# Kernel tuning notes

Measured on AMD Instinct MI355X. Metric: run time of the kernel, lower is better.

Reference implementation:

```python
import jax, jax.numpy as jnp
import numpy as np

CHUNK = 4        # rows per split
IN_F = 72        # 4*6*3 flattened chunk
OUT_F = 1800     # linear output, viewed as (180,5,2)


def setup_inputs() -> dict:
    key = jax.random.key(0)
    k1, k2, k3 = jax.random.split(key, 3)
    N = 262144  # multiple of 4, so torch's zero-padding of the last chunk is a no-op
    x = jax.random.normal(k1, (N, 6, 3), dtype=jnp.float32)
    W = jax.random.normal(k2, (OUT_F, IN_F), dtype=jnp.float32) * (1.0 / np.sqrt(IN_F))
    b = jax.random.normal(k3, (OUT_F,), dtype=jnp.float32) * 0.01
    return {"x": x, "W": W, "b": b}


def reference(x, W, b):
    # Original: for each split of 4 rows of [6,3], pad to (4,6,3), flatten to 72,
    # Linear(72,1800) + ReLU, view (180,5,2); concatenate all chunks.
    # Vectorized: reshape to [n_chunks, 72] and do one batched GEMM.
    n = x.shape[0]
    n_chunks = -(-n // CHUNK)
    pad = n_chunks * CHUNK - n
    if pad:
        x = jnp.concatenate([x, jnp.zeros((pad, 6, 3), dtype=x.dtype)], axis=0)
    flat = x.reshape(n_chunks, IN_F)                       # [C, 72]
    h = jax.nn.relu(jnp.einsum('ci,oi->co', flat, W) + b)  # [C, 1800]
    # torch returns torch.split(cat, 180): equivalent to the concatenated array
    return h.reshape(n_chunks * 180, 5, 2)
```

## Files before the change

### kernel.cpp

```cpp
#include <hip/hip_runtime.h>
#include <hip/hip_bf16.h>


typedef __bf16 bf16;
typedef bf16  bf16x4 __attribute__((ext_vector_type(4)));
typedef bf16  bf16x8 __attribute__((ext_vector_type(8)));
typedef float f32x4  __attribute__((ext_vector_type(4)));

#define KDIM 72
#define LDK  104
#define NDIM 1800
#define BM   64
#define BN   64

__global__ __launch_bounds__(256, 4)
void edges_mlp_kernel(const float* __restrict__ A,
                      const float* __restrict__ W,
                      const float* __restrict__ bias,
                      float* __restrict__ out)
{
    __shared__ bf16 As[BM][LDK];
    __shared__ bf16 Bs[BN][LDK];

    const int t  = threadIdx.x;
    const int n0 = blockIdx.x * BN;
    const int m0 = blockIdx.y * BM;

    for (int idx = t; idx < BM * 3 * 2; idx += 256) {
        int half = idx / (BM * 3);
        int rem  = idx % (BM * 3);
        int r    = rem / 3;
        int part = rem % 3;
        char* base = half ? (char*)&Bs[r][0] : (char*)&As[r][0];
        *(uint4*)(base + KDIM * 2 + part * 16) = make_uint4(0u, 0u, 0u, 0u);
    }

    const float4* A4 = (const float4*)(A + (size_t)m0 * KDIM);
    for (int i = t; i < BM * (KDIM / 4); i += 256) {
        int m = i / (KDIM / 4);
        int q = i % (KDIM / 4);
        float4 v = A4[i];
        bf16x4 h = { (bf16)v.x, (bf16)v.y, (bf16)v.z, (bf16)v.w };
        *(bf16x4*)&As[m][q * 4] = h;
    }
    for (int i = t; i < BN * (KDIM / 4); i += 256) {
        int n = i / (KDIM / 4);
        int q = i % (KDIM / 4);
        int gn = n0 + n;
        float4 v = make_float4(0.f, 0.f, 0.f, 0.f);
        if (gn < NDIM) v = *(const float4*)(W + (size_t)gn * KDIM + q * 4);
        bf16x4 h = { (bf16)v.x, (bf16)v.y, (bf16)v.z, (bf16)v.w };
        *(bf16x4*)&Bs[n][q * 4] = h;
    }
    __syncthreads();

    const int wave = t >> 6;
    const int lane = t & 63;
    const int lrow = lane & 15;
    const int lkb  = (lane >> 4) * 8;

    f32x4 acc[4] = { {0,0,0,0}, {0,0,0,0}, {0,0,0,0}, {0,0,0,0} };

    #pragma unroll
    for (int ks = 0; ks < 3; ++ks) {
        bf16x8 a = *(const bf16x8*)&As[wave * 16 + lrow][ks * 32 + lkb];
        #pragma unroll
        for (int nt = 0; nt < 4; ++nt) {
            bf16x8 bf = *(const bf16x8*)&Bs[nt * 16 + lrow][ks * 32 + lkb];
            acc[nt] = __builtin_amdgcn_mfma_f32_16x16x32_bf16(a, bf, acc[nt], 0, 0, 0);
        }
    }

    const int orow0 = m0 + wave * 16 + (lane >> 4) * 4;
    #pragma unroll
    for (int nt = 0; nt < 4; ++nt) {
        int col = n0 + nt * 16 + lrow;
        if (col < NDIM) {
            float bv = bias[col];
            #pragma unroll
            for (int r = 0; r < 4; ++r) {
                float v = fmaxf(acc[nt][r] + bv, 0.0f);
                __builtin_nontemporal_store(v, &out[(size_t)(orow0 + r) * NDIM + col]);
            }
        }
    }
}

extern "C" void kernel_launch(void* const* d_in, const int* in_sizes, int n_in,
                              void* d_out, int out_size, void* d_ws, size_t ws_size,
                              hipStream_t stream) {
    const float* x = (const float*)d_in[0];
    const float* W = (const float*)d_in[1];
    const float* b = (const float*)d_in[2];
    float* out = (float*)d_out;

    const int chunks = in_sizes[0] / KDIM;
    dim3 grid((NDIM + BN - 1) / BN, chunks / BM);
    edges_mlp_kernel<<<grid, 256, 0, stream>>>(x, W, b, out);
}
```

Before: 640.1 us.

## Make blocks persistent over M tiles with W fragments held in registers

Each block now loads its 64-column slice of W into shared memory once, keeps the B fragments and bias in registers, and loops over M tiles with a stride of NSEG rows of blocks. The A tile is read straight from global memory into MFMA fragments instead of being staged through LDS. This removes the repeated W conversion, the LDS traffic and the per-tile sync. In exchange it hardcodes MTILES=1024, which ties the kernel to N=262144, and the grid shrinks to 29x64 blocks.

```diff
diff --git a/kernel.cpp b/kernel.cpp
--- a/kernel.cpp
+++ b/kernel.cpp
@@ -7,11 +7,10 @@
 typedef bf16  bf16x8 __attribute__((ext_vector_type(8)));
 typedef float f32x4  __attribute__((ext_vector_type(4)));
 
-#define KDIM 72
-#define LDK  104
-#define NDIM 1800
-#define BM   64
-#define BN   64
+#define KDIM   72
+#define NDIM   1800
+#define MTILES 1024
+#define NSEG   64
 
 __global__ __launch_bounds__(256, 4)
 void edges_mlp_kernel(const float* __restrict__ A,
@@ -19,33 +18,17 @@
                       const float* __restrict__ bias,
                       float* __restrict__ out)
 {
-    __shared__ bf16 As[BM][LDK];
-    __shared__ bf16 Bs[BN][LDK];
+    __shared__ bf16 Bs[64][104];
 
     const int t  = threadIdx.x;
-    const int n0 = blockIdx.x * BN;
-    const int m0 = blockIdx.y * BM;
+    const int n0 = blockIdx.x * 64;
 
-    for (int idx = t; idx < BM * 3 * 2; idx += 256) {
-        int half = idx / (BM * 3);
-        int rem  = idx % (BM * 3);
-        int r    = rem / 3;
-        int part = rem % 3;
-        char* base = half ? (char*)&Bs[r][0] : (char*)&As[r][0];
-        *(uint4*)(base + KDIM * 2 + part * 16) = make_uint4(0u, 0u, 0u, 0u);
+    for (int idx = t; idx < 64 * 3; idx += 256) {
+        int r = idx / 3, p = idx % 3;
+        *(uint4*)((char*)&Bs[r][0] + KDIM * 2 + p * 16) = make_uint4(0u, 0u, 0u, 0u);
     }
-
-    const float4* A4 = (const float4*)(A + (size_t)m0 * KDIM);
-    for (int i = t; i < BM * (KDIM / 4); i += 256) {
-        int m = i / (KDIM / 4);
-        int q = i % (KDIM / 4);
-        float4 v = A4[i];
-        bf16x4 h = { (bf16)v.x, (bf16)v.y, (bf16)v.z, (bf16)v.w };
-        *(bf16x4*)&As[m][q * 4] = h;
-    }
-    for (int i = t; i < BN * (KDIM / 4); i += 256) {
-        int n = i / (KDIM / 4);
-        int q = i % (KDIM / 4);
+    for (int i = t; i < 64 * 18; i += 256) {
+        int n = i / 18, q = i % 18;
         int gn = n0 + n;
         float4 v = make_float4(0.f, 0.f, 0.f, 0.f);
         if (gn < NDIM) v = *(const float4*)(W + (size_t)gn * KDIM + q * 4);
@@ -57,30 +40,65 @@
     const int wave = t >> 6;
     const int lane = t & 63;
     const int lrow = lane & 15;
-    const int lkb  = (lane >> 4) * 8;
+    const int hi   = lane >> 4;
 
-    f32x4 acc[4] = { {0,0,0,0}, {0,0,0,0}, {0,0,0,0}, {0,0,0,0} };
+    bf16x8 bfrag[3][4];
+    #pragma unroll
+    for (int ks = 0; ks < 3; ++ks)
+        #pragma unroll
+        for (int nt = 0; nt < 4; ++nt)
+            bfrag[ks][nt] = *(const bf16x8*)&Bs[nt * 16 + lrow][ks * 32 + hi * 8];
 
-    #pragma unroll
-    for (int ks = 0; ks < 3; ++ks) {
-        bf16x8 a = *(const bf16x8*)&As[wave * 16 + lrow][ks * 32 + lkb];
-        #pragma unroll
-        for (int nt = 0; nt < 4; ++nt) {
-            bf16x8 bf = *(const bf16x8*)&Bs[nt * 16 + lrow][ks * 32 + lkb];
-            acc[nt] = __builtin_amdgcn_mfma_f32_16x16x32_bf16(a, bf, acc[nt], 0, 0, 0);
-        }
-    }
-
-    const int orow0 = m0 + wave * 16 + (lane >> 4) * 4;
+    float bv[4];
     #pragma unroll
     for (int nt = 0; nt < 4; ++nt) {
         int col = n0 + nt * 16 + lrow;
-        if (col < NDIM) {
-            float bv = bias[col];
+        bv[nt] = (col < NDIM) ? bias[col] : 0.f;
+    }
+
+    const int arow_in_tile = wave * 16 + lrow;
+
+    for (int mt = blockIdx.y; mt < MTILES; mt += NSEG) {
+        const size_t m0 = (size_t)mt * 64;
+        const float* arow = A + (m0 + arow_in_tile) * KDIM;
+
+        bf16x8 afrag[3];
+        #pragma unroll
+        for (int ks = 0; ks < 3; ++ks) {
+            const int k0 = ks * 32 + hi * 8;
+            float av[8];
+            if (k0 < KDIM) {
+                float4 u0 = *(const float4*)(arow + k0);
+                float4 u1 = *(const float4*)(arow + k0 + 4);
+                av[0] = u0.x; av[1] = u0.y; av[2] = u0.z; av[3] = u0.w;
+                av[4] = u1.x; av[5] = u1.y; av[6] = u1.z; av[7] = u1.w;
+            } else {
+                #pragma unroll
+                for (int j = 0; j < 8; ++j) av[j] = 0.f;
+            }
+            bf16x8 h;
             #pragma unroll
-            for (int r = 0; r < 4; ++r) {
-                float v = fmaxf(acc[nt][r] + bv, 0.0f);
-                __builtin_nontemporal_store(v, &out[(size_t)(orow0 + r) * NDIM + col]);
+            for (int j = 0; j < 8; ++j) h[j] = (bf16)av[j];
+            afrag[ks] = h;
+        }
+
+        f32x4 acc[4] = { {0,0,0,0}, {0,0,0,0}, {0,0,0,0}, {0,0,0,0} };
+        #pragma unroll
+        for (int ks = 0; ks < 3; ++ks)
+            #pragma unroll
+            for (int nt = 0; nt < 4; ++nt)
+                acc[nt] = __builtin_amdgcn_mfma_f32_16x16x32_bf16(afrag[ks], bfrag[ks][nt], acc[nt], 0, 0, 0);
+
+        const size_t orow0 = m0 + wave * 16 + hi * 4;
+        #pragma unroll
+        for (int nt = 0; nt < 4; ++nt) {
+            int col = n0 + nt * 16 + lrow;
+            if (col < NDIM) {
+                #pragma unroll
+                for (int r = 0; r < 4; ++r) {
+                    float v = fmaxf(acc[nt][r] + bv[nt], 0.0f);
+                    __builtin_nontemporal_store(v, &out[(orow0 + r) * NDIM + col]);
+                }
             }
         }
     }
@@ -94,7 +112,6 @@
     const float* b = (const float*)d_in[2];
     float* out = (float*)d_out;
 
-    const int chunks = in_sizes[0] / KDIM;
-    dim3 grid((NDIM + BN - 1) / BN, chunks / BM);
+    dim3 grid((NDIM + 63) / 64, NSEG);
     edges_mlp_kernel<<<grid, 256, 0, stream>>>(x, W, b, out);
 }
```

After: 708.0 us. 1.11x slower.
